# Kernel optimization log

Hardware: AMD Instinct MI355X
Metric: run time of the kernel (lower is better)

Reference implementation:

```python
import jax, jax.numpy as jnp
import numpy as np

INPUT_DIM, HIDDEN, CB_DIM, CB_SIZE = 768, 512, 256, 512
COMMIT_W = 1.0


def setup_inputs() -> dict:
    key = jax.random.key(0)
    ks = jax.random.split(key, 10)
    def lin(k, fan_in, fan_out):
        lim = 1.0 / np.sqrt(fan_in)
        return jax.random.uniform(k, (fan_in, fan_out), jnp.float32, -lim, lim)
    return {
        "x": jax.random.normal(ks[0], (32, 2048, INPUT_DIM), jnp.float32),
        "W1": lin(ks[1], INPUT_DIM, HIDDEN),
        "b1": jnp.zeros((HIDDEN,), jnp.float32),
        "W2": lin(ks[2], HIDDEN, CB_DIM),
        "b2": jnp.zeros((CB_DIM,), jnp.float32),
        "codebook": jax.random.normal(ks[3], (CB_SIZE, CB_DIM), jnp.float32),
        "W3": lin(ks[4], CB_DIM, HIDDEN),
        "b3": jnp.zeros((HIDDEN,), jnp.float32),
        "W4": lin(ks[5], HIDDEN, INPUT_DIM),
        "b4": jnp.zeros((INPUT_DIM,), jnp.float32),
    }


def reference(x, W1, b1, W2, b2, codebook, W3, b3, W4, b4):
    # encoder MLP: [b, n, 768] -> [b, n, 256]
    h = jax.nn.relu(jnp.einsum('bnd,dh->bnh', x, W1) + b1)
    z = jnp.einsum('bnh,hc->bnc', h, W2) + b2

    # VQ: squared-L2 distance to codebook, argmin, gather
    # d(z, c) = ||z||^2 - 2 z.c + ||c||^2  (||z||^2 constant over argmin, omitted)
    dots = jnp.einsum('bnc,kc->bnk', z, codebook)          # [b, n, K]
    c_sq = jnp.sum(codebook * codebook, axis=-1)            # [K]
    indices = jnp.argmin(c_sq - 2.0 * dots, axis=-1)        # [b, n] int
    q = codebook[indices]                                   # [b, n, 256] gather

    # straight-through estimator + commitment loss
    quantized = z + jax.lax.stop_gradient(q - z)
    commit_loss = COMMIT_W * jnp.mean((z - jax.lax.stop_gradient(q)) ** 2)

    # decoder MLP: [b, n, 256] -> [b, n, 768]
    h2 = jax.nn.relu(jnp.einsum('bnc,ch->bnh', quantized, W3) + b3)
    recon = jnp.einsum('bnh,hd->bnd', h2, W4) + b4
    return recon, indices.astype(jnp.int32), commit_loss
```

## Files before the change

### kernel.cpp

```cpp
#include <hip/hip_runtime.h>

typedef unsigned short u16;
typedef unsigned int   u32;
typedef __attribute__((ext_vector_type(8))) short short8;
typedef __attribute__((ext_vector_type(4))) float f32x4;

#define NTOK 65536
#define IND  768
#define HID  512
#define CBD  256
#define CBS  512

#define OUT_IDX_OFF   ((size_t)NTOK * IND)
#define OUT_LOSS_OFF  (OUT_IDX_OFF + NTOK)

#define OFF_H      ((size_t)0)
#define OFF_Z      ((size_t)134217728)
#define OFF_W1H    ((size_t)201326592)
#define OFF_W1L    ((size_t)202113024)
#define OFF_W2H    ((size_t)202899456)
#define OFF_W2L    ((size_t)203161600)
#define OFF_CBH    ((size_t)203423744)
#define OFF_CBL    ((size_t)203685888)
#define OFF_CSQ    ((size_t)203948032)
#define OFF_PART   ((size_t)0)
#define OFF_TABLE  ((size_t)8388608)
#define OFF_ZSQ    ((size_t)9961472)
#define OFF_IDX    ((size_t)10223616)
#define OFF_FLAGS  ((size_t)10485760)
#define OFF_CNT    ((size_t)10747904)

__device__ __forceinline__ u16 f2bf(float f) {
    u32 u = __float_as_uint(f);
    return (u16)((u + 0x7fffu + ((u >> 16) & 1u)) >> 16);
}
__device__ __forceinline__ float bf2f(u16 h) {
    return __uint_as_float(((u32)h) << 16);
}

__global__ __launch_bounds__(256) void cbsplit(
    const float* __restrict__ cb, u16* __restrict__ hi, u16* __restrict__ lo,
    float* __restrict__ csq)
{
    int c = blockIdx.x, t = threadIdx.x;
    float v = cb[(size_t)c * CBD + t];
    u16 h = f2bf(v); u16 l = f2bf(v - bf2f(h));
    hi[(size_t)c * CBD + t] = h; lo[(size_t)c * CBD + t] = l;
    __shared__ float red[256];
    red[t] = v * v; __syncthreads();
    for (int s = 128; s; s >>= 1) { if (t < s) red[t] += red[t + s]; __syncthreads(); }
    if (!t) csq[c] = red[0];
}

__global__ __launch_bounds__(256) void wsplit(
    const float* __restrict__ W, u16* __restrict__ hi, u16* __restrict__ lo,
    int K, int N)
{
    int n = blockIdx.x;
    for (int k = threadIdx.x; k < K; k += 256) {
        float v = W[(size_t)k * N + n];
        u16 h = f2bf(v); u16 l = f2bf(v - bf2f(h));
        hi[(size_t)n * K + k] = h; lo[(size_t)n * K + k] = l;
    }
}

template<int AMODE, int EPI>
__global__ __launch_bounds__(256, 2) void gemm3(
    const float* __restrict__ Af, const u32* __restrict__ Apk,
    const u16* __restrict__ Bhi, const u16* __restrict__ Blo,
    const float* __restrict__ bias,
    u32* __restrict__ Opk, float* __restrict__ Opart,
    int M, int N, int K)
{
    __shared__ u16 lds[4 * 128 * 40];
    u16* sAh = lds;
    u16* sAl = lds + 5120;
    u16* sBh = lds + 10240;
    u16* sBl = lds + 15360;
    const int tid  = threadIdx.x;
    const int m0 = blockIdx.y * 128, n0 = blockIdx.x * 128;
    const int w = tid >> 6, lane = tid & 63, quad = lane >> 4, l15 = lane & 15;
    const int wm = (w & 1) * 64, wn = (w >> 1) * 64;

    f32x4 acc[4][4] = {};

    for (int k0 = 0; k0 < K; k0 += 32) {
        __syncthreads();
        if (AMODE == 0) {
            #pragma unroll
            for (int s = 0; s < 4; ++s) {
                int slot = tid + s * 256;
                int m = slot >> 3, kg = (slot & 7) << 2;
                float4 v = *(const float4*)(Af + (size_t)(m0 + m) * K + k0 + kg);
                u16 h0 = f2bf(v.x), h1 = f2bf(v.y), h2 = f2bf(v.z), h3 = f2bf(v.w);
                ushort4 hv = {h0, h1, h2, h3};
                ushort4 lv = {f2bf(v.x - bf2f(h0)), f2bf(v.y - bf2f(h1)),
                              f2bf(v.z - bf2f(h2)), f2bf(v.w - bf2f(h3))};
                *(ushort4*)&sAh[m * 40 + kg] = hv;
                *(ushort4*)&sAl[m * 40 + kg] = lv;
            }
        } else {
            #pragma unroll
            for (int s = 0; s < 4; ++s) {
                int slot = tid + s * 256;
                int m = slot >> 3, ke = (slot & 7) << 2;
                uint4 u = *(const uint4*)(Apk + (size_t)(m0 + m) * K + k0 + ke);
                ushort4 hv = {(u16)(u.x & 0xffff), (u16)(u.y & 0xffff),
                              (u16)(u.z & 0xffff), (u16)(u.w & 0xffff)};
                ushort4 lv = {(u16)(u.x >> 16), (u16)(u.y >> 16),
                              (u16)(u.z >> 16), (u16)(u.w >> 16)};
                *(ushort4*)&sAh[m * 40 + ke] = hv;
                *(ushort4*)&sAl[m * 40 + ke] = lv;
            }
        }
        #pragma unroll
        for (int s = 0; s < 4; ++s) {
            int slot = tid + s * 256;
            int n = (slot & 511) >> 2, ku = slot & 3;
            const u16* src = (slot < 512) ? Bhi : Blo;
            u16* dst = (slot < 512) ? sBh : sBl;
            uint4 u = *(const uint4*)(src + (size_t)(n0 + n) * K + k0 + ku * 8);
            *(uint4*)&dst[n * 40 + ku * 8] = u;
        }
        __syncthreads();

        short8 ah[4], al[4], bh[4], bl[4];
        const int ko = quad * 8;
        #pragma unroll
        for (int i = 0; i < 4; ++i) {
            int ar = wm + i * 16 + l15;
            int br = wn + i * 16 + l15;
            ah[i] = *(const short8*)&sAh[ar * 40 + ko];
            al[i] = *(const short8*)&sAl[ar * 40 + ko];
            bh[i] = *(const short8*)&sBh[br * 40 + ko];
            bl[i] = *(const short8*)&sBl[br * 40 + ko];
        }
        #pragma unroll
        for (int i = 0; i < 4; ++i)
            #pragma unroll
            for (int j = 0; j < 4; ++j) {
                acc[i][j] = __builtin_amdgcn_mfma_f32_16x16x32_bf16(ah[i], bh[j], acc[i][j], 0, 0, 0);
                acc[i][j] = __builtin_amdgcn_mfma_f32_16x16x32_bf16(ah[i], bl[j], acc[i][j], 0, 0, 0);
                acc[i][j] = __builtin_amdgcn_mfma_f32_16x16x32_bf16(al[i], bh[j], acc[i][j], 0, 0, 0);
            }
    }

    if (EPI <= 1) {
        float bn[4];
        #pragma unroll
        for (int j = 0; j < 4; ++j) bn[j] = bias[n0 + wn + j * 16 + l15];
        #pragma unroll
        for (int i = 0; i < 4; ++i)
            #pragma unroll
            for (int r = 0; r < 4; ++r) {
                int row = m0 + wm + i * 16 + quad * 4 + r;
                #pragma unroll
                for (int j = 0; j < 4; ++j) {
                    float v = acc[i][j][r] + bn[j];
                    if (EPI == 0) v = fmaxf(v, 0.f);
                    u16 h = f2bf(v); u16 l = f2bf(v - bf2f(h));
                    Opk[(size_t)row * N + n0 + wn + j * 16 + l15] = (u32)h | ((u32)l << 16);
                }
            }
    } else {
        float cs[4]; int cidx[4];
        #pragma unroll
        for (int j = 0; j < 4; ++j) {
            cidx[j] = n0 + wn + j * 16 + l15;
            cs[j] = bias[cidx[j]];
        }
        const int nparts = gridDim.x * 2;
        const int pslot  = blockIdx.x * 2 + (w >> 1);
        #pragma unroll
        for (int i = 0; i < 4; ++i)
            #pragma unroll
            for (int r = 0; r < 4; ++r) {
                int row = m0 + wm + i * 16 + quad * 4 + r;
                float d1 = 3.4e38f, d2 = 3.4e38f; int i1 = 0x7fffffff;
                #pragma unroll
                for (int j = 0; j < 4; ++j) {
                    float v = fmaf(-2.0f, acc[i][j][r], cs[j]);
                    if (v < d1) { d2 = d1; d1 = v; i1 = cidx[j]; }
                    else d2 = fminf(d2, v);
                }
                #pragma unroll
                for (int mm = 1; mm < 16; mm <<= 1) {
                    float od1 = __shfl_xor(d1, mm, 64);
                    float od2 = __shfl_xor(d2, mm, 64);
                    int   oi1 = __shfl_xor(i1, mm, 64);
                    if (od1 < d1 || (od1 == d1 && oi1 < i1)) { d2 = fminf(d1, od2); d1 = od1; i1 = oi1; }
                    else d2 = fminf(d2, od1);
                }
                if (l15 == 0) {
                    float4 o = {d1, d2, __int_as_float(i1), 0.f};
                    *(float4*)&Opart[((size_t)row * nparts + pslot) * 4] = o;
                }
            }
    }
}

__global__ __launch_bounds__(256) void zsq_pk(
    const u32* __restrict__ Zpk, float* __restrict__ zsq)
{
    int tok = blockIdx.x * 4 + (threadIdx.x >> 6);
    int lane = threadIdx.x & 63;
    uint4 u = *(const uint4*)(Zpk + (size_t)tok * CBD + lane * 4);
    float z0 = bf2f((u16)(u.x & 0xffff)) + bf2f((u16)(u.x >> 16));
    float z1 = bf2f((u16)(u.y & 0xffff)) + bf2f((u16)(u.y >> 16));
    float z2 = bf2f((u16)(u.z & 0xffff)) + bf2f((u16)(u.z >> 16));
    float z3 = bf2f((u16)(u.w & 0xffff)) + bf2f((u16)(u.w >> 16));
    float s = z0 * z0 + z1 * z1 + z2 * z2 + z3 * z3;
    #pragma unroll
    for (int off = 32; off; off >>= 1) s += __shfl_down(s, off, 64);
    if (!lane) zsq[tok] = s;
}

__global__ __launch_bounds__(256) void vq_reduce(
    const float* __restrict__ part, const float* __restrict__ zsq,
    float* __restrict__ out_idx, int* __restrict__ idx_i,
    int* __restrict__ cnt, float* __restrict__ accum, int* __restrict__ flags)
{
    int tok = blockIdx.x * 256 + threadIdx.x;
    float d1 = 3.4e38f, d2 = 3.4e38f; int i1 = 0x7fffffff;
    #pragma unroll
    for (int nb = 0; nb < 8; ++nb) {
        float4 p = *(const float4*)&part[((size_t)tok * 8 + nb) * 4];
        float pd1 = p.x, pd2 = p.y; int pi1 = __float_as_int(p.z);
        if (pd1 < d1 || (pd1 == d1 && pi1 < i1)) { d2 = fminf(d1, pd2); d1 = pd1; i1 = pi1; }
        else d2 = fminf(d2, pd1);
    }
    out_idx[tok] = (float)i1;
    idx_i[tok] = i1;
    if (d2 - d1 < 0.01f) {
        int p = atomicAdd(cnt, 1);
        if (p >= 0 && p < NTOK) flags[p] = tok;
    }
    float c = zsq[tok] + d1;
    __shared__ float red[256];
    red[threadIdx.x] = c; __syncthreads();
    for (int s = 128; s; s >>= 1) { if (threadIdx.x < s) red[threadIdx.x] += red[threadIdx.x + s]; __syncthreads(); }
    if (!threadIdx.x) atomicAdd(accum, red[0]);
}

__global__ __launch_bounds__(256) void fixup(
    const int* __restrict__ cnt, const int* __restrict__ flags,
    const float* __restrict__ x, const float* __restrict__ W1, const float* __restrict__ b1,
    const float* __restrict__ W2, const float* __restrict__ b2,
    const float* __restrict__ cb, const float* __restrict__ csq,
    int* __restrict__ idx_i, float* __restrict__ out_idx)
{
    __shared__ float xs[8][IND];
    __shared__ float hs[8][HID];
    __shared__ float zs[8][CBD];
    __shared__ float bd_s[4][8];
    __shared__ int   bi_s[4][8];
    __shared__ int   tok_s[8];

    int n = cnt[0]; if (n > NTOK) n = NTOK; if (n < 0) n = 0;
    const int t = threadIdx.x;
    const int nb = (n + 7) >> 3;

    for (int ib = blockIdx.x; ib < nb; ib += gridDim.x) {
        const int base = ib * 8;
        if (t < 8) {
            int fi = base + t; if (fi > n - 1) fi = n - 1;
            tok_s[t] = flags[fi];
        }
        __syncthreads();

        #pragma unroll
        for (int s = 0; s < 6; ++s) {
            int slot = t + s * 256;
            int tt = slot / 192, c4 = slot - tt * 192;
            *(float4*)&xs[tt][c4 * 4] =
                *(const float4*)(x + (size_t)tok_s[tt] * IND + c4 * 4);
        }
        __syncthreads();

        {
            const int tg = t >> 7;
            const int j0 = (t & 127) * 4;
            float a[4][4];
            float4 bb = *(const float4*)(b1 + j0);
            #pragma unroll
            for (int ti = 0; ti < 4; ++ti) {
                a[ti][0] = bb.x; a[ti][1] = bb.y; a[ti][2] = bb.z; a[ti][3] = bb.w;
            }
            for (int k4 = 0; k4 < IND / 4; ++k4) {
                float4 xv[4];
                #pragma unroll
                for (int ti = 0; ti < 4; ++ti)
                    xv[ti] = *(const float4*)&xs[tg * 4 + ti][k4 * 4];
                #pragma unroll
                for (int kk = 0; kk < 4; ++kk) {
                    float4 wv = *(const float4*)(W1 + (size_t)(k4 * 4 + kk) * HID + j0);
                    #pragma unroll
                    for (int ti = 0; ti < 4; ++ti) {
                        float xk = (kk == 0) ? xv[ti].x : (kk == 1) ? xv[ti].y
                                 : (kk == 2) ? xv[ti].z : xv[ti].w;
                        a[ti][0] = fmaf(xk, wv.x, a[ti][0]);
                        a[ti][1] = fmaf(xk, wv.y, a[ti][1]);
                        a[ti][2] = fmaf(xk, wv.z, a[ti][2]);
                        a[ti][3] = fmaf(xk, wv.w, a[ti][3]);
                    }
                }
            }
            #pragma unroll
            for (int ti = 0; ti < 4; ++ti) {
                float4 o = {fmaxf(a[ti][0], 0.f), fmaxf(a[ti][1], 0.f),
                            fmaxf(a[ti][2], 0.f), fmaxf(a[ti][3], 0.f)};
                *(float4*)&hs[tg * 4 + ti][j0] = o;
            }
        }
        __syncthreads();

        {
            const int tg = t >> 6;
            const int c0 = (t & 63) * 4;
            float az[2][4];
            float4 bz = *(const float4*)(b2 + c0);
            #pragma unroll
            for (int ti = 0; ti < 2; ++ti) {
                az[ti][0] = bz.x; az[ti][1] = bz.y; az[ti][2] = bz.z; az[ti][3] = bz.w;
            }
            for (int k4 = 0; k4 < HID / 4; ++k4) {
                float4 hv[2];
                #pragma unroll
                for (int ti = 0; ti < 2; ++ti)
                    hv[ti] = *(const float4*)&hs[tg * 2 + ti][k4 * 4];
                #pragma unroll
                for (int kk = 0; kk < 4; ++kk) {
                    float4 wv = *(const float4*)(W2 + (size_t)(k4 * 4 + kk) * CBD + c0);
                    #pragma unroll
                    for (int ti = 0; ti < 2; ++ti) {
                        float hk = (kk == 0) ? hv[ti].x : (kk == 1) ? hv[ti].y
                                 : (kk == 2) ? hv[ti].z : hv[ti].w;
                        az[ti][0] = fmaf(hk, wv.x, az[ti][0]);
                        az[ti][1] = fmaf(hk, wv.y, az[ti][1]);
                        az[ti][2] = fmaf(hk, wv.z, az[ti][2]);
                        az[ti][3] = fmaf(hk, wv.w, az[ti][3]);
                    }
                }
            }
            #pragma unroll
            for (int ti = 0; ti < 2; ++ti) {
                float4 o = {az[ti][0], az[ti][1], az[ti][2], az[ti][3]};
                *(float4*)&zs[tg * 2 + ti][c0] = o;
            }
        }
        __syncthreads();

        {
            const int wv = t >> 6, l = t & 63;
            float4 zv[8];
            #pragma unroll
            for (int tt = 0; tt < 8; ++tt) zv[tt] = *(const float4*)&zs[tt][l * 4];
            float bd[8]; int bi[8];
            #pragma unroll
            for (int tt = 0; tt < 8; ++tt) { bd[tt] = 3.4e38f; bi[tt] = 0x7fffffff; }
            for (int cc = 0; cc < 128; ++cc) {
                int c = wv * 128 + cc;
                float4 cv = *(const float4*)(cb + (size_t)c * CBD + l * 4);
                float cs = csq[c];
                #pragma unroll
                for (int tt = 0; tt < 8; ++tt) {
                    float p = zv[tt].x * cv.x + zv[tt].y * cv.y + zv[tt].z * cv.z + zv[tt].w * cv.w;
                    #pragma unroll
                    for (int mm = 32; mm; mm >>= 1) p += __shfl_xor(p, mm, 64);
                    float d = cs - 2.f * p;
                    if (d < bd[tt]) { bd[tt] = d; bi[tt] = c; }
                }
            }
            if (l == 0) {
                #pragma unroll
                for (int tt = 0; tt < 8; ++tt) { bd_s[wv][tt] = bd[tt]; bi_s[wv][tt] = bi[tt]; }
            }
        }
        __syncthreads();

        if (t < 8) {
            const int tt = t;
            float d = bd_s[0][tt]; int i = bi_s[0][tt];
            #pragma unroll
            for (int wv = 1; wv < 4; ++wv) {
                float od = bd_s[wv][tt]; int oi = bi_s[wv][tt];
                if (od < d || (od == d && oi < i)) { d = od; i = oi; }
            }
            if (base + tt < n) {
                int tok = tok_s[tt];
                idx_i[tok] = i; out_idx[tok] = (float)i;
            }
        }
        __syncthreads();
    }
}

__global__ __launch_bounds__(256) void table_pre(
    const float* __restrict__ cb, const float* __restrict__ W3,
    const float* __restrict__ b3, const float* __restrict__ W4,
    const float* __restrict__ b4, float* __restrict__ table)
{
    __shared__ float crow[CBD];
    __shared__ float h2[HID];
    const int c = blockIdx.x;
    const int t = threadIdx.x;
    crow[t] = cb[(size_t)c * CBD + t];
    __syncthreads();
    #pragma unroll
    for (int s = 0; s < 2; ++s) {
        int j = t + s * 256;
        float acc = b3[j];
        for (int k = 0; k < CBD; ++k) acc = fmaf(crow[k], W3[(size_t)k * HID + j], acc);
        h2[j] = fmaxf(acc, 0.f);
    }
    __syncthreads();
    #pragma unroll
    for (int s = 0; s < 3; ++s) {
        int j = t + s * 256;
        float acc = b4[j];
        for (int k = 0; k < HID; ++k) acc = fmaf(h2[k], W4[(size_t)k * IND + j], acc);
        table[(size_t)c * IND + j] = acc;
    }
}

__global__ __launch_bounds__(256) void gather_kernel(
    const int* __restrict__ idx, const float* __restrict__ table,
    float* __restrict__ out)
{
    unsigned i = blockIdx.x * 256u + threadIdx.x;
    unsigned tok = i / 192u;
    unsigned c = i - tok * 192u;
    int id = idx[tok];
    ((float4*)out)[i] = ((const float4*)table)[(size_t)id * 192 + c];
}

__global__ void finalize_kernel(const float* __restrict__ accum,
                                float* __restrict__ out_loss)
{
    out_loss[0] = accum[0] * (1.0f / 16777216.0f);
}

extern "C" void kernel_launch(void* const* d_in, const int* in_sizes, int n_in,
                              void* d_out, int out_size, void* d_ws, size_t ws_size,
                              hipStream_t stream) {
    const float* x  = (const float*)d_in[0];
    const float* W1 = (const float*)d_in[1];
    const float* b1 = (const float*)d_in[2];
    const float* W2 = (const float*)d_in[3];
    const float* b2 = (const float*)d_in[4];
    const float* cb = (const float*)d_in[5];
    const float* W3 = (const float*)d_in[6];
    const float* b3 = (const float*)d_in[7];
    const float* W4 = (const float*)d_in[8];
    const float* b4 = (const float*)d_in[9];

    char* ws = (char*)d_ws;
    u32*  Hpk   = (u32*)(ws + OFF_H);
    u32*  Zpk   = (u32*)(ws + OFF_Z);
    u16*  W1h   = (u16*)(ws + OFF_W1H);
    u16*  W1l   = (u16*)(ws + OFF_W1L);
    u16*  W2h   = (u16*)(ws + OFF_W2H);
    u16*  W2l   = (u16*)(ws + OFF_W2L);
    u16*  CBh   = (u16*)(ws + OFF_CBH);
    u16*  CBl   = (u16*)(ws + OFF_CBL);
    float* csq  = (float*)(ws + OFF_CSQ);
    float* part = (float*)(ws + OFF_PART);
    float* table = (float*)(ws + OFF_TABLE);
    float* zsq  = (float*)(ws + OFF_ZSQ);
    int*   idx_i = (int*)(ws + OFF_IDX);
    int*   flags = (int*)(ws + OFF_FLAGS);
    int*   cnt   = (int*)(ws + OFF_CNT);
    float* accum = (float*)(ws + OFF_CNT + 4);

    float* out      = (float*)d_out;
    float* out_idx  = out + OUT_IDX_OFF;
    float* out_loss = out + OUT_LOSS_OFF;

    cbsplit<<<CBS, 256, 0, stream>>>(cb, CBh, CBl, csq);
    wsplit<<<HID, 256, 0, stream>>>(W1, W1h, W1l, IND, HID);
    wsplit<<<CBD, 256, 0, stream>>>(W2, W2h, W2l, HID, CBD);

    gemm3<0, 0><<<dim3(HID / 128, NTOK / 128), 256, 0, stream>>>(
        x, (const u32*)nullptr, W1h, W1l, b1, Hpk, (float*)nullptr, NTOK, HID, IND);
    gemm3<1, 1><<<dim3(CBD / 128, NTOK / 128), 256, 0, stream>>>(
        (const float*)nullptr, Hpk, W2h, W2l, b2, Zpk, (float*)nullptr, NTOK, CBD, HID);

    hipMemsetAsync(cnt, 0, 8, stream);

    zsq_pk<<<NTOK / 4, 256, 0, stream>>>(Zpk, zsq);

    gemm3<1, 2><<<dim3(CBS / 128, NTOK / 128), 256, 0, stream>>>(
        (const float*)nullptr, Zpk, CBh, CBl, csq, (u32*)nullptr, part, NTOK, CBS, CBD);

    table_pre<<<CBS, 256, 0, stream>>>(cb, W3, b3, W4, b4, table);

    vq_reduce<<<NTOK / 256, 256, 0, stream>>>(part, zsq, out_idx, idx_i, cnt, accum, flags);

    fixup<<<1024, 256, 0, stream>>>(cnt, flags, x, W1, b1, W2, b2, cb, csq, idx_i, out_idx);

    gather_kernel<<<(NTOK * (IND / 4)) / 256, 256, 0, stream>>>(idx_i, table, out);

    finalize_kernel<<<1, 1, 0, stream>>>(accum, out_loss);
}
```

Before: 947.3 us.

## Use k-chunked LDS layout and remap workgroups across XCDs in gemm3

Shared-memory tiles change from row-major with a padded stride of 40 to a layout split into k-chunks of 8, each chunk a contiguous plane of rows with its own padding. MFMA operand reads then touch consecutive 16-byte rows, which should reduce LDS bank conflicts. Workgroup IDs are also remapped so consecutive logical tiles go to the same XCD, aiming for better L2 reuse on MI355X's chiplet layout. The remap assumes the grid size divides by 8, and the partial-slot index now follows the remapped column.

```diff
diff --git a/kernel.cpp b/kernel.cpp
--- a/kernel.cpp
+++ b/kernel.cpp
@@ -64,6 +64,9 @@
     }
 }
 
+#define CHS 1040
+#define PLN (4 * CHS)
+
 template<int AMODE, int EPI>
 __global__ __launch_bounds__(256, 2) void gemm3(
     const float* __restrict__ Af, const u32* __restrict__ Apk,
@@ -72,13 +75,20 @@
     u32* __restrict__ Opk, float* __restrict__ Opart,
     int M, int N, int K)
 {
-    __shared__ u16 lds[4 * 128 * 40];
+    __shared__ u16 lds[4 * PLN];
     u16* sAh = lds;
-    u16* sAl = lds + 5120;
-    u16* sBh = lds + 10240;
-    u16* sBl = lds + 15360;
+    u16* sAl = lds + PLN;
+    u16* sBh = lds + 2 * PLN;
+    u16* sBl = lds + 3 * PLN;
     const int tid  = threadIdx.x;
-    const int m0 = blockIdx.y * 128, n0 = blockIdx.x * 128;
+
+    const int nwg = gridDim.x * gridDim.y;
+    const int hw  = blockIdx.y * gridDim.x + blockIdx.x;
+    const int logical = (hw & 7) * (nwg >> 3) + (hw >> 3);
+    const int bx = logical % gridDim.x;
+    const int by = logical / gridDim.x;
+
+    const int m0 = by * 128, n0 = bx * 128;
     const int w = tid >> 6, lane = tid & 63, quad = lane >> 4, l15 = lane & 15;
     const int wm = (w & 1) * 64, wn = (w >> 1) * 64;
 
@@ -91,26 +101,28 @@
             for (int s = 0; s < 4; ++s) {
                 int slot = tid + s * 256;
                 int m = slot >> 3, kg = (slot & 7) << 2;
+                int c = kg >> 3, off = kg & 7;
                 float4 v = *(const float4*)(Af + (size_t)(m0 + m) * K + k0 + kg);
                 u16 h0 = f2bf(v.x), h1 = f2bf(v.y), h2 = f2bf(v.z), h3 = f2bf(v.w);
                 ushort4 hv = {h0, h1, h2, h3};
                 ushort4 lv = {f2bf(v.x - bf2f(h0)), f2bf(v.y - bf2f(h1)),
                               f2bf(v.z - bf2f(h2)), f2bf(v.w - bf2f(h3))};
-                *(ushort4*)&sAh[m * 40 + kg] = hv;
-                *(ushort4*)&sAl[m * 40 + kg] = lv;
+                *(ushort4*)&sAh[c * CHS + m * 8 + off] = hv;
+                *(ushort4*)&sAl[c * CHS + m * 8 + off] = lv;
             }
         } else {
             #pragma unroll
             for (int s = 0; s < 4; ++s) {
                 int slot = tid + s * 256;
                 int m = slot >> 3, ke = (slot & 7) << 2;
+                int c = ke >> 3, off = ke & 7;
                 uint4 u = *(const uint4*)(Apk + (size_t)(m0 + m) * K + k0 + ke);
                 ushort4 hv = {(u16)(u.x & 0xffff), (u16)(u.y & 0xffff),
                               (u16)(u.z & 0xffff), (u16)(u.w & 0xffff)};
                 ushort4 lv = {(u16)(u.x >> 16), (u16)(u.y >> 16),
                               (u16)(u.z >> 16), (u16)(u.w >> 16)};
-                *(ushort4*)&sAh[m * 40 + ke] = hv;
-                *(ushort4*)&sAl[m * 40 + ke] = lv;
+                *(ushort4*)&sAh[c * CHS + m * 8 + off] = hv;
+                *(ushort4*)&sAl[c * CHS + m * 8 + off] = lv;
             }
         }
         #pragma unroll
@@ -120,20 +132,20 @@
             const u16* src = (slot < 512) ? Bhi : Blo;
             u16* dst = (slot < 512) ? sBh : sBl;
             uint4 u = *(const uint4*)(src + (size_t)(n0 + n) * K + k0 + ku * 8);
-            *(uint4*)&dst[n * 40 + ku * 8] = u;
+            *(uint4*)&dst[ku * CHS + n * 8] = u;
         }
         __syncthreads();
 
         short8 ah[4], al[4], bh[4], bl[4];
-        const int ko = quad * 8;
+        const int kc = quad * CHS;
         #pragma unroll
         for (int i = 0; i < 4; ++i) {
             int ar = wm + i * 16 + l15;
             int br = wn + i * 16 + l15;
-            ah[i] = *(const short8*)&sAh[ar * 40 + ko];
-            al[i] = *(const short8*)&sAl[ar * 40 + ko];
-            bh[i] = *(const short8*)&sBh[br * 40 + ko];
-            bl[i] = *(const short8*)&sBl[br * 40 + ko];
+            ah[i] = *(const short8*)&sAh[kc + ar * 8];
+            al[i] = *(const short8*)&sAl[kc + ar * 8];
+            bh[i] = *(const short8*)&sBh[kc + br * 8];
+            bl[i] = *(const short8*)&sBl[kc + br * 8];
         }
         #pragma unroll
         for (int i = 0; i < 4; ++i)
@@ -170,7 +182,7 @@
             cs[j] = bias[cidx[j]];
         }
         const int nparts = gridDim.x * 2;
-        const int pslot  = blockIdx.x * 2 + (w >> 1);
+        const int pslot  = bx * 2 + (w >> 1);
         #pragma unroll
         for (int i = 0; i < 4; ++i)
             #pragma unroll
```

New measurement: 918.0 us. 3.1% less time.
